# Kernel optimization log

Measured on AMD Instinct MI355X. Metric: run time of the kernel, lower is better.

The kernel has to match this reference:

```python
import jax, jax.numpy as jnp
import numpy as np

K = 3
OFFSET_SCALE = 0.25
GN_GROUPS = 8
GN_EPS = 1e-5


def setup_inputs() -> dict:
    key = jax.random.key(0)
    k1, k2, k3 = jax.random.split(key, 3)
    N, C, H, W = 4, 128, 96, 96
    Cout = 128
    x = jax.random.normal(k1, (N, C, H, W), dtype=jnp.float32)
    # offset head: small random weights so offsets are modest (tanh tames anyway)
    w_head = jax.random.normal(k2, (3, C, 3, 3), dtype=jnp.float32) * 0.05
    b_head = jnp.zeros((3,), dtype=jnp.float32)
    # kaiming-ish scale for the deform conv weight: sqrt(2 / fan_out)
    w_dcn = jax.random.normal(k3, (Cout, C, 3, 3), dtype=jnp.float32) * np.sqrt(2.0 / (Cout * 9))
    gn_gamma = jnp.ones((Cout,), dtype=jnp.float32)
    gn_beta = jnp.zeros((Cout,), dtype=jnp.float32)
    return {"x": x, "w_head": w_head, "b_head": b_head, "w_dcn": w_dcn,
            "gn_gamma": gn_gamma, "gn_beta": gn_beta}


def _conv3x3(x, w, b):
    y = jax.lax.conv_general_dilated(
        x, w, window_strides=(1, 1), padding=((1, 1), (1, 1)),
        dimension_numbers=("NCHW", "OIHW", "NCHW"))
    return y + b[None, :, None, None]


def _deform_sample(xn, py, px):
    # xn: (C,H,W); py/px: (9,H,W) absolute sampling coords (y=row, x=col)
    C, H, W = xn.shape
    y0 = jnp.floor(py).astype(jnp.int32)
    x0 = jnp.floor(px).astype(jnp.int32)
    fy = py - y0
    fx = px - x0
    xf = xn.reshape(C, H * W)

    def corner(yi, xi, wgt):
        valid = (yi >= 0) & (yi < H) & (xi >= 0) & (xi < W)
        idx = jnp.clip(yi, 0, H - 1) * W + jnp.clip(xi, 0, W - 1)  # (9,H,W)
        v = xf[:, idx.reshape(-1)].reshape(C, *idx.shape)  # (C,9,H,W)
        return v * (wgt * valid)[None]

    return (corner(y0, x0, (1 - fy) * (1 - fx))
            + corner(y0, x0 + 1, (1 - fy) * fx)
            + corner(y0 + 1, x0, fy * (1 - fx))
            + corner(y0 + 1, x0 + 1, fy * fx))


def reference(x, w_head, b_head, w_dcn, gn_gamma, gn_beta):
    N, C, H, W = x.shape
    Cout = w_dcn.shape[0]
    stride, pad, dil = 1, 1, 1

    head = _conv3x3(x, w_head, b_head)                 # (N,3,H,W)
    dx, dy, m = head[:, :1], head[:, 1:2], head[:, 2:3]
    mask = jax.nn.sigmoid(m)                           # (N,1,H,W) broadcast over 9 taps
    dx = OFFSET_SCALE * jnp.tanh(dx)
    dy = OFFSET_SCALE * jnp.tanh(dy)

    # serpentine 18-channel offsets, mmcv layout: (oy, ox) pairs per kernel tap
    z = jnp.zeros_like(dx)
    offs = jnp.concatenate(
        [z, z, z, dy, z, -dy, dx, z, z, z, -dx, z, dx, dy, dx, -dy, -dx, dy], axis=1)
    offs = offs.reshape(N, 9, 2, H, W)
    oy, ox = offs[:, :, 0], offs[:, :, 1]              # (N,9,H,W)

    ky = jnp.arange(9) // 3
    kx = jnp.arange(9) % 3
    base_y = (jnp.arange(H) * stride - pad)[None, :, None] + (ky * dil)[:, None, None]
    base_x = (jnp.arange(W) * stride - pad)[None, None, :] + (kx * dil)[:, None, None]
    py = base_y[None] + oy                             # (N,9,H,W)
    px = base_x[None] + ox

    sampled = jax.vmap(_deform_sample)(x, py, px)      # (N,C,9,H,W)
    sampled = sampled * mask[:, None]                  # modulated

    y = jnp.einsum('nckhw,ock->nohw', sampled, w_dcn.reshape(Cout, C, 9))

    # GroupNorm(8, Cout) + ReLU
    G = min(GN_GROUPS, Cout)
    yg = y.reshape(N, G, Cout // G, H, W)
    mu = yg.mean(axis=(2, 3, 4), keepdims=True)
    var = yg.var(axis=(2, 3, 4), keepdims=True)
    yn = ((yg - mu) * jax.lax.rsqrt(var + GN_EPS)).reshape(N, Cout, H, W)
    yn = yn * gn_gamma[None, :, None, None] + gn_beta[None, :, None, None]
    return jax.nn.relu(yn)
```

## Files before the change

kernel.cpp:

```cpp
#include <hip/hip_runtime.h>
#include <hip/hip_bf16.h>
#include <math.h>

#define NB   4
#define CIN  128
#define HH   96
#define WW   96
#define HWN  (HH*WW)
#define NHW  (NB*HWN)
#define COUT 128
#define KW   9
#define KDIM (CIN*KW)
#define GSZ  16
#define PXB  32
#define NBLK (NHW/PXB)

typedef __attribute__((ext_vector_type(8))) short bf16x8;
typedef __attribute__((ext_vector_type(4))) float f32x4;

#define OFF_WAH   0
#define OFF_DX    147456
#define OFF_DY    184320
#define OFF_MASK  221184
#define OFF_GN    258048
#define OFF_MAP   258240
#define OFF_PAIR  258496

__device__ __forceinline__ ushort f2bf(float f) {
    union { float f; uint u; } v; v.f = f;
    uint r = v.u + 0x7fffu + ((v.u >> 16) & 1u);
    return (ushort)(r >> 16);
}
__device__ __forceinline__ float bf2f(ushort h) {
    union { uint u; float f; } v; v.u = ((uint)h) << 16;
    return v.f;
}

__device__ __forceinline__ void barrier_keep_vm() {
    asm volatile("s_waitcnt lgkmcnt(0)\n\ts_barrier" ::: "memory");
}

__global__ __launch_bounds__(256) void pre_kernel(const float* __restrict__ x,
                                                  const float* __restrict__ w_head,
                                                  const float* __restrict__ b_head,
                                                  const float* __restrict__ wd,
                                                  ushort* __restrict__ wah,
                                                  float* __restrict__ dxv,
                                                  float* __restrict__ dyv,
                                                  float* __restrict__ maskv,
                                                  float* __restrict__ gn_part,
                                                  int* __restrict__ map,
                                                  int* __restrict__ pairB) {
    __shared__ float wl[3456];
    __shared__ float sp[4][64][3];
    const int b = blockIdx.x, t = threadIdx.x;

    if (b >= 576) {
        const int bb = b - 576;
        int i = bb * 256 + t;
        {
            int e  = i & 7;
            int l  = (i >> 3) & 63;
            int ot = (i >> 9) & 7;
            int q  = (i >> 12) & 3;
            int k  = i >> 14;
            int o  = ot * 16 + (l & 15);
            int c  = q * 32 + (l >> 4) * 8 + e;
            wah[i] = f2bf(wd[o * KDIM + c * KW + k]);
        }
        if (bb == 0 && t < 128) gn_part[t] = 0.f;
        if (bb == 0 && t < 64) {
            int l = t;
            bf16x8 A1 = {}, B1 = {}, A2 = {}, B2 = {};
            if ((l >> 4) == 0) {
                A1[0] = (short)f2bf((float)((l & 15) + 1));
                B1[0] = (short)f2bf(1.0f);
                A2[0] = (short)f2bf(1.0f);
                B2[0] = (short)f2bf((float)((l & 15) + 1));
            }
            f32x4 d1 = {0.f,0.f,0.f,0.f}, d2 = {0.f,0.f,0.f,0.f};
            d1 = __builtin_amdgcn_mfma_f32_16x16x32_bf16(A1, B1, d1, 0, 0, 0);
            d2 = __builtin_amdgcn_mfma_f32_16x16x32_bf16(A2, B2, d2, 0, 0, 0);
#pragma unroll
            for (int r = 0; r < 4; ++r) {
                int m = (int)(d1[r] + 0.5f) - 1;
                int n = (int)(d2[r] + 0.5f) - 1;
                map[l * 4 + r] = (m << 4) | n;
            }
        }
        if (bb == 1 && t < 64) {
            int l = t;
            union { bf16x8 v; short a[8]; } B;
#pragma unroll
            for (int e = 0; e < 8; ++e) {
                float val = (float)(1u << (((l >> 4) * 8 + e) & 31));
                B.a[e] = (short)f2bf(val);
            }
#pragma unroll
            for (int s = 0; s < 32; ++s) {
                union { bf16x8 v; short a[8]; } A;
#pragma unroll
                for (int e = 0; e < 8; ++e) A.a[e] = 0;
                if ((l >> 4) == (s >> 3)) A.a[s & 7] = (short)f2bf(1.0f);
                f32x4 d = {0.f, 0.f, 0.f, 0.f};
                d = __builtin_amdgcn_mfma_f32_16x16x32_bf16(A.v, B.v, d, 0, 0, 0);
                float v0 = d[0];
                if (l == 0 && v0 > 0.f) {
                    int ex; frexpf(v0, &ex);
                    int j = ex - 1;
                    if (j >= 0 && j < 32) pairB[j] = s;
                }
            }
        }
        return;
    }

    for (int i = t; i < 3456; i += 256) {
        int j = i / KDIM, r = i - j * KDIM;
        wl[r * 3 + j] = w_head[i];
    }
    __syncthreads();

    int lane = t & 63, cg = t >> 6;
    int p = b * 64 + lane;
    int n = p / HWN, hw = p % HWN;
    int h = hw / WW, w = hw % WW;

    int   offs[9];
    float msk[9];
#pragma unroll
    for (int ky = 0; ky < 3; ky++)
#pragma unroll
        for (int kx = 0; kx < 3; kx++) {
            int yy = h - 1 + ky, xx = w - 1 + kx;
            bool ok = (yy >= 0) && (yy < HH) && (xx >= 0) && (xx < WW);
            int yc = min(max(yy, 0), HH - 1), xc = min(max(xx, 0), WW - 1);
            offs[ky * 3 + kx] = yc * WW + xc;
            msk[ky * 3 + kx] = ok ? 1.f : 0.f;
        }

    float a0 = 0.f, a1 = 0.f, a2 = 0.f;
    const float* xn = x + (size_t)n * CIN * HWN;
    for (int c = cg * 32; c < cg * 32 + 32; c++) {
        const float* xc = xn + c * HWN;
        const float* wc = &wl[c * 27];
#pragma unroll
        for (int kk = 0; kk < 9; kk++) {
            float v = xc[offs[kk]] * msk[kk];
            a0 = fmaf(v, wc[kk * 3 + 0], a0);
            a1 = fmaf(v, wc[kk * 3 + 1], a1);
            a2 = fmaf(v, wc[kk * 3 + 2], a2);
        }
    }
    sp[cg][lane][0] = a0; sp[cg][lane][1] = a1; sp[cg][lane][2] = a2;
    __syncthreads();
    if (t < 64) {
        float b0 = sp[0][t][0] + sp[1][t][0] + sp[2][t][0] + sp[3][t][0] + b_head[0];
        float b1 = sp[0][t][1] + sp[1][t][1] + sp[2][t][1] + sp[3][t][1] + b_head[1];
        float b2 = sp[0][t][2] + sp[1][t][2] + sp[2][t][2] + sp[3][t][2] + b_head[2];
        int pp = b * 64 + t;
        dxv[pp]   = 0.25f * tanhf(b0);
        dyv[pp]   = 0.25f * tanhf(b1);
        maskv[pp] = 1.f / (1.f + expf(-b2));
    }
}

__global__ __launch_bounds__(256) void dcn_kernel(const float* __restrict__ x,
                                                  const ushort* __restrict__ wah,
                                                  const float* __restrict__ dxv,
                                                  const float* __restrict__ dyv,
                                                  const float* __restrict__ maskv,
                                                  const int* __restrict__ map,
                                                  const int* __restrict__ pairB,
                                                  float* __restrict__ out,
                                                  float* __restrict__ gn_part) {
    __shared__ __attribute__((aligned(16))) ushort sBh[2][4 * PXB * 8];
    __shared__ float sMask[PXB];
    __shared__ float gred[16];

    const int t = threadIdx.x;
    const int lane = t & 63;
    const int wv = t >> 6;
    const int lg = lane >> 4;
    const int ml = lane & 15;
    const int pix = t & 31;
    const int sg  = t >> 5;

    int b = blockIdx.x;
    int nb = (b & 7) * (NBLK / 8) + (b >> 3);
    const int p0  = nb * PXB;
    const int n   = p0 / HWN;
    const int hw0 = p0 % HWN;
    const float* xn = x + (size_t)n * CIN * HWN;

    if (t < PXB) sMask[t] = maskv[p0 + t];
    if (t < 16) gred[t] = 0.f;

    const float dxl = dxv[p0 + pix];
    const float dyl = dyv[p0 + pix];
    const int hme = (hw0 + pix) / WW;
    const int wme = (hw0 + pix) % WW;

    int chn[4];
#pragma unroll
    for (int e = 0; e < 4; ++e) chn[e] = pairB[sg * 4 + e] & 31;

    f32x4 acc[2][2];
#pragma unroll
    for (int i = 0; i < 2; i++)
#pragma unroll
        for (int j = 0; j < 2; j++) acc[i][j] = (f32x4){0.f, 0.f, 0.f, 0.f};

    const int oyc[9] = {0, 0, 0, 1, 0, -1, 1, 1, -1};
    const int oxc[9] = {0, 1, -1, 0, 0, 0, 1, -1, 1};
    const int ncl[9] = {1, 2, 2, 2, 1, 2, 4, 4, 4};

    int aa[4]; float wq[4];
    float raw[4][4];
    bf16x8 An0, An1;

    {
        float py = (float)(hme - 1), px = (float)(wme - 1);
        float fy0 = floorf(py), fx0 = floorf(px);
        int y0 = (int)fy0, x0 = (int)fx0;
        float fy = py - fy0, fx = px - fx0;
#pragma unroll
        for (int j = 0; j < 4; ++j) {
            int yy = y0 + (j >> 1), xx = x0 + (j & 1);
            float wb = ((j >> 1) ? fy : 1.f - fy) * ((j & 1) ? fx : 1.f - fx);
            bool ok = (yy >= 0) && (yy < HH) && (xx >= 0) && (xx < WW);
            aa[j] = min(max(yy, 0), HH - 1) * WW + min(max(xx, 0), WW - 1);
            wq[j] = ok ? wb : 0.f;
        }
#pragma unroll
        for (int e = 0; e < 4; ++e) raw[e][0] = xn[(size_t)chn[e] * HWN + aa[0]];
        const size_t abase = (size_t)(wv * 2) * 512 + lane * 8;
        An0 = *(const bf16x8*)(wah + abase);
        An1 = *(const bf16x8*)(wah + abase + 512);
    }

#pragma unroll
    for (int j = 0; j < 36; ++j) {
        const int k = j >> 2;
        const int NC = ncl[k];
        bf16x8 Ah0 = An0, Ah1 = An1;
        union { short4 v; ushort u[4]; } hv;
#pragma unroll
        for (int e = 0; e < 4; ++e) {
            float s = raw[e][0] * wq[0];
            if (NC >= 2) s += raw[e][1] * wq[1];
            if (NC == 4) s += raw[e][2] * wq[2] + raw[e][3] * wq[3];
            hv.u[e] = f2bf(s);
        }
        const int wbase = ((sg >> 1) * PXB + pix) * 8 + (sg & 1) * 4;
        *(short4*)&sBh[j & 1][wbase] = hv.v;
        if (j < 35) {
            const int jn = j + 1, kn = jn >> 2, qn = jn & 3;
            if (qn == 0) {
                const int ky = kn / 3, kx = kn - ky * 3;
                float py = (float)(hme - 1 + ky) + (float)oyc[kn] * dxl;
                float px = (float)(wme - 1 + kx) + (float)oxc[kn] * dyl;
                float fy0 = floorf(py), fx0 = floorf(px);
                int y0 = (int)fy0, x0 = (int)fx0;
                float fy = py - fy0, fx = px - fx0;
#pragma unroll
                for (int jj = 0; jj < 4; ++jj) {
                    int yy = y0 + (jj >> 1), xx = x0 + (jj & 1);
                    float wb = ((jj >> 1) ? fy : 1.f - fy) * ((jj & 1) ? fx : 1.f - fx);
                    bool ok = (yy >= 0) && (yy < HH) && (xx >= 0) && (xx < WW);
                    aa[jj] = min(max(yy, 0), HH - 1) * WW + min(max(xx, 0), WW - 1);
                    wq[jj] = ok ? wb : 0.f;
                }
                if (ncl[kn] == 2 && oxc[kn] == 0) { aa[1] = aa[2]; wq[1] = wq[2]; }
            }
            const int NCn = ncl[kn];
            const int ccn = qn * 32;
#pragma unroll
            for (int e = 0; e < 4; ++e) {
                const float* xc = xn + (size_t)(ccn + chn[e]) * HWN;
                raw[e][0] = xc[aa[0]];
                if (NCn >= 2) raw[e][1] = xc[aa[1]];
                if (NCn == 4) { raw[e][2] = xc[aa[2]]; raw[e][3] = xc[aa[3]]; }
            }
            const size_t abase = (size_t)((kn * 4 + qn) * 8 + wv * 2) * 512 + lane * 8;
            An0 = *(const bf16x8*)(wah + abase);
            An1 = *(const bf16x8*)(wah + abase + 512);
        }
        barrier_keep_vm();
#pragma unroll
        for (int pt = 0; pt < 2; ++pt) {
            const int rbase = (lg * PXB + pt * 16 + ml) * 8;
            bf16x8 Bh = *(const bf16x8*)&sBh[j & 1][rbase];
            acc[0][pt] = __builtin_amdgcn_mfma_f32_16x16x32_bf16(Ah0, Bh, acc[0][pt], 0, 0, 0);
            acc[1][pt] = __builtin_amdgcn_mfma_f32_16x16x32_bf16(Ah1, Bh, acc[1][pt], 0, 0, 0);
        }
    }

    int4 mn4 = *(const int4*)&map[lane * 4];
    int mn[4] = {mn4.x, mn4.y, mn4.z, mn4.w};
    float s1g[2] = {0.f, 0.f}, s2g[2] = {0.f, 0.f};
#pragma unroll
    for (int ot = 0; ot < 2; ++ot) {
        int otile = wv * 32 + ot * 16;
#pragma unroll
        for (int pt = 0; pt < 2; ++pt) {
#pragma unroll
            for (int r = 0; r < 4; ++r) {
                int m = mn[r] >> 4, nn2 = mn[r] & 15;
                int p = pt * 16 + nn2;
                float v = acc[ot][pt][r] * sMask[p];
                s1g[ot] += v;
                s2g[ot] += v * v;
                out[((size_t)n * COUT + otile + m) * HWN + hw0 + p] = v;
            }
        }
    }
#pragma unroll
    for (int ot = 0; ot < 2; ++ot) {
        int g = wv * 2 + ot;
        atomicAdd(&gred[g * 2 + 0], s1g[ot]);
        atomicAdd(&gred[g * 2 + 1], s2g[ot]);
    }
    __syncthreads();
    if (t < 8) {
        atomicAdd(&gn_part[n * 8 + t],      gred[t * 2 + 0]);
        atomicAdd(&gn_part[64 + n * 8 + t], gred[t * 2 + 1]);
    }
}

__global__ __launch_bounds__(256) void gn_apply(float* __restrict__ out,
                                                const float* __restrict__ gn_part,
                                                const float* __restrict__ gamma,
                                                const float* __restrict__ beta) {
    int i4 = blockIdx.x * 256 + threadIdx.x;
    size_t e = (size_t)i4 * 4;
    int og = (int)(e / HWN);
    int n = og >> 7, o = og & 127;
    int s = n * 8 + (o >> 4);
    const float cnt = (float)GSZ * (float)HWN;
    float s1 = gn_part[s], s2 = gn_part[64 + s];
    float mu = s1 / cnt;
    float var = s2 / cnt - mu * mu;
    float inv = rsqrtf(var + 1e-5f);
    float ga = gamma[o] * inv;
    float be = beta[o] - mu * ga;
    float4 v = *(float4*)(out + e);
    v.x = fmaxf(fmaf(v.x, ga, be), 0.f);
    v.y = fmaxf(fmaf(v.y, ga, be), 0.f);
    v.z = fmaxf(fmaf(v.z, ga, be), 0.f);
    v.w = fmaxf(fmaf(v.w, ga, be), 0.f);
    *(float4*)(out + e) = v;
}

extern "C" void kernel_launch(void* const* d_in, const int* in_sizes, int n_in,
                              void* d_out, int out_size, void* d_ws, size_t ws_size,
                              hipStream_t stream) {
    const float* x       = (const float*)d_in[0];
    const float* w_head  = (const float*)d_in[1];
    const float* b_head  = (const float*)d_in[2];
    const float* w_dcn   = (const float*)d_in[3];
    const float* gamma   = (const float*)d_in[4];
    const float* beta    = (const float*)d_in[5];
    float* out = (float*)d_out;
    float* ws  = (float*)d_ws;

    ushort* wah    = (ushort*)(ws + OFF_WAH);
    float* dxv     = ws + OFF_DX;
    float* dyv     = ws + OFF_DY;
    float* maskv   = ws + OFF_MASK;
    float* gn_part = ws + OFF_GN;
    int*   map     = (int*)(ws + OFF_MAP);
    int*   pairB   = (int*)(ws + OFF_PAIR);

    pre_kernel<<<1152, 256, 0, stream>>>(x, w_head, b_head, w_dcn, wah,
                                         dxv, dyv, maskv, gn_part, map, pairB);
    dcn_kernel<<<NBLK, 256, 0, stream>>>(x, wah, dxv, dyv, maskv, map, pairB, out, gn_part);
    gn_apply<<<(NB * COUT * HWN) / 4 / 256, 256, 0, stream>>>(out, gn_part, gamma, beta);
}
```

Before: 181.4 us.

## Fuse offset-head conv into DCN kernel and halve pixel tile to 16

Moves the 3-channel offset/mask head convolution out of the pre-kernel and into the deformable conv kernel, so each block computes dx, dy and mask for its own 16 pixels in shared memory. This removes the global round-trip of the offset buffers and the dependency between the two kernels. The pixel tile per block drops from 32 to 16, which doubles the block count and halves the MFMA work per block. In exchange, every block reloads the full head weights into shared memory and does an extra reduction across 16 channel groups.

```diff
diff --git a/kernel.cpp b/kernel.cpp
--- a/kernel.cpp
+++ b/kernel.cpp
@@ -12,16 +12,13 @@
 #define KW   9
 #define KDIM (CIN*KW)
 #define GSZ  16
-#define PXB  32
+#define PXB  16
 #define NBLK (NHW/PXB)
 
 typedef __attribute__((ext_vector_type(8))) short bf16x8;
 typedef __attribute__((ext_vector_type(4))) float f32x4;
 
 #define OFF_WAH   0
-#define OFF_DX    147456
-#define OFF_DY    184320
-#define OFF_MASK  221184
 #define OFF_GN    258048
 #define OFF_MAP   258240
 #define OFF_PAIR  258496
@@ -31,160 +28,95 @@
     uint r = v.u + 0x7fffu + ((v.u >> 16) & 1u);
     return (ushort)(r >> 16);
 }
-__device__ __forceinline__ float bf2f(ushort h) {
-    union { uint u; float f; } v; v.u = ((uint)h) << 16;
-    return v.f;
-}
 
 __device__ __forceinline__ void barrier_keep_vm() {
     asm volatile("s_waitcnt lgkmcnt(0)\n\ts_barrier" ::: "memory");
 }
 
-__global__ __launch_bounds__(256) void pre_kernel(const float* __restrict__ x,
-                                                  const float* __restrict__ w_head,
-                                                  const float* __restrict__ b_head,
-                                                  const float* __restrict__ wd,
+__global__ __launch_bounds__(256) void pre_kernel(const float* __restrict__ wd,
                                                   ushort* __restrict__ wah,
-                                                  float* __restrict__ dxv,
-                                                  float* __restrict__ dyv,
-                                                  float* __restrict__ maskv,
                                                   float* __restrict__ gn_part,
                                                   int* __restrict__ map,
                                                   int* __restrict__ pairB) {
-    __shared__ float wl[3456];
-    __shared__ float sp[4][64][3];
     const int b = blockIdx.x, t = threadIdx.x;
-
-    if (b >= 576) {
-        const int bb = b - 576;
-        int i = bb * 256 + t;
-        {
-            int e  = i & 7;
-            int l  = (i >> 3) & 63;
-            int ot = (i >> 9) & 7;
-            int q  = (i >> 12) & 3;
-            int k  = i >> 14;
-            int o  = ot * 16 + (l & 15);
-            int c  = q * 32 + (l >> 4) * 8 + e;
-            wah[i] = f2bf(wd[o * KDIM + c * KW + k]);
-        }
-        if (bb == 0 && t < 128) gn_part[t] = 0.f;
-        if (bb == 0 && t < 64) {
-            int l = t;
-            bf16x8 A1 = {}, B1 = {}, A2 = {}, B2 = {};
-            if ((l >> 4) == 0) {
-                A1[0] = (short)f2bf((float)((l & 15) + 1));
-                B1[0] = (short)f2bf(1.0f);
-                A2[0] = (short)f2bf(1.0f);
-                B2[0] = (short)f2bf((float)((l & 15) + 1));
-            }
-            f32x4 d1 = {0.f,0.f,0.f,0.f}, d2 = {0.f,0.f,0.f,0.f};
-            d1 = __builtin_amdgcn_mfma_f32_16x16x32_bf16(A1, B1, d1, 0, 0, 0);
-            d2 = __builtin_amdgcn_mfma_f32_16x16x32_bf16(A2, B2, d2, 0, 0, 0);
-#pragma unroll
-            for (int r = 0; r < 4; ++r) {
-                int m = (int)(d1[r] + 0.5f) - 1;
-                int n = (int)(d2[r] + 0.5f) - 1;
-                map[l * 4 + r] = (m << 4) | n;
-            }
-        }
-        if (bb == 1 && t < 64) {
-            int l = t;
-            union { bf16x8 v; short a[8]; } B;
-#pragma unroll
-            for (int e = 0; e < 8; ++e) {
-                float val = (float)(1u << (((l >> 4) * 8 + e) & 31));
-                B.a[e] = (short)f2bf(val);
-            }
-#pragma unroll
-            for (int s = 0; s < 32; ++s) {
-                union { bf16x8 v; short a[8]; } A;
-#pragma unroll
-                for (int e = 0; e < 8; ++e) A.a[e] = 0;
-                if ((l >> 4) == (s >> 3)) A.a[s & 7] = (short)f2bf(1.0f);
-                f32x4 d = {0.f, 0.f, 0.f, 0.f};
-                d = __builtin_amdgcn_mfma_f32_16x16x32_bf16(A.v, B.v, d, 0, 0, 0);
-                float v0 = d[0];
-                if (l == 0 && v0 > 0.f) {
-                    int ex; frexpf(v0, &ex);
-                    int j = ex - 1;
-                    if (j >= 0 && j < 32) pairB[j] = s;
-                }
-            }
-        }
-        return;
-    }
-
-    for (int i = t; i < 3456; i += 256) {
-        int j = i / KDIM, r = i - j * KDIM;
-        wl[r * 3 + j] = w_head[i];
-    }
-    __syncthreads();
-
-    int lane = t & 63, cg = t >> 6;
-    int p = b * 64 + lane;
-    int n = p / HWN, hw = p % HWN;
-    int h = hw / WW, w = hw % WW;
-
-    int   offs[9];
-    float msk[9];
-#pragma unroll
-    for (int ky = 0; ky < 3; ky++)
-#pragma unroll
-        for (int kx = 0; kx < 3; kx++) {
-            int yy = h - 1 + ky, xx = w - 1 + kx;
-            bool ok = (yy >= 0) && (yy < HH) && (xx >= 0) && (xx < WW);
-            int yc = min(max(yy, 0), HH - 1), xc = min(max(xx, 0), WW - 1);
-            offs[ky * 3 + kx] = yc * WW + xc;
-            msk[ky * 3 + kx] = ok ? 1.f : 0.f;
-        }
-
-    float a0 = 0.f, a1 = 0.f, a2 = 0.f;
-    const float* xn = x + (size_t)n * CIN * HWN;
-    for (int c = cg * 32; c < cg * 32 + 32; c++) {
-        const float* xc = xn + c * HWN;
-        const float* wc = &wl[c * 27];
-#pragma unroll
-        for (int kk = 0; kk < 9; kk++) {
-            float v = xc[offs[kk]] * msk[kk];
-            a0 = fmaf(v, wc[kk * 3 + 0], a0);
-            a1 = fmaf(v, wc[kk * 3 + 1], a1);
-            a2 = fmaf(v, wc[kk * 3 + 2], a2);
-        }
-    }
-    sp[cg][lane][0] = a0; sp[cg][lane][1] = a1; sp[cg][lane][2] = a2;
-    __syncthreads();
-    if (t < 64) {
-        float b0 = sp[0][t][0] + sp[1][t][0] + sp[2][t][0] + sp[3][t][0] + b_head[0];
-        float b1 = sp[0][t][1] + sp[1][t][1] + sp[2][t][1] + sp[3][t][1] + b_head[1];
-        float b2 = sp[0][t][2] + sp[1][t][2] + sp[2][t][2] + sp[3][t][2] + b_head[2];
-        int pp = b * 64 + t;
-        dxv[pp]   = 0.25f * tanhf(b0);
-        dyv[pp]   = 0.25f * tanhf(b1);
-        maskv[pp] = 1.f / (1.f + expf(-b2));
+    int i = b * 256 + t;
+    {
+        int e  = i & 7;
+        int l  = (i >> 3) & 63;
+        int ot = (i >> 9) & 7;
+        int q  = (i >> 12) & 3;
+        int k  = i >> 14;
+        int o  = ot * 16 + (l & 15);
+        int c  = q * 32 + (l >> 4) * 8 + e;
+        wah[i] = f2bf(wd[o * KDIM + c * KW + k]);
+    }
+    if (b == 0 && t < 128) gn_part[t] = 0.f;
+    if (b == 0 && t < 64) {
+        int l = t;
+        bf16x8 A1 = {}, B1 = {}, A2 = {}, B2 = {};
+        if ((l >> 4) == 0) {
+            A1[0] = (short)f2bf((float)((l & 15) + 1));
+            B1[0] = (short)f2bf(1.0f);
+            A2[0] = (short)f2bf(1.0f);
+            B2[0] = (short)f2bf((float)((l & 15) + 1));
+        }
+        f32x4 d1 = {0.f,0.f,0.f,0.f}, d2 = {0.f,0.f,0.f,0.f};
+        d1 = __builtin_amdgcn_mfma_f32_16x16x32_bf16(A1, B1, d1, 0, 0, 0);
+        d2 = __builtin_amdgcn_mfma_f32_16x16x32_bf16(A2, B2, d2, 0, 0, 0);
+#pragma unroll
+        for (int r = 0; r < 4; ++r) {
+            int m = (int)(d1[r] + 0.5f) - 1;
+            int n = (int)(d2[r] + 0.5f) - 1;
+            map[l * 4 + r] = (m << 4) | n;
+        }
+    }
+    if (b == 1 && t < 64) {
+        int l = t;
+        union { bf16x8 v; short a[8]; } B;
+#pragma unroll
+        for (int e = 0; e < 8; ++e) {
+            float val = (float)(1u << (((l >> 4) * 8 + e) & 31));
+            B.a[e] = (short)f2bf(val);
+        }
+#pragma unroll
+        for (int s = 0; s < 32; ++s) {
+            union { bf16x8 v; short a[8]; } A;
+#pragma unroll
+            for (int e = 0; e < 8; ++e) A.a[e] = 0;
+            if ((l >> 4) == (s >> 3)) A.a[s & 7] = (short)f2bf(1.0f);
+            f32x4 d = {0.f, 0.f, 0.f, 0.f};
+            d = __builtin_amdgcn_mfma_f32_16x16x32_bf16(A.v, B.v, d, 0, 0, 0);
+            float v0 = d[0];
+            if (l == 0 && v0 > 0.f) {
+                int ex; frexpf(v0, &ex);
+                int j = ex - 1;
+                if (j >= 0 && j < 32) pairB[j] = s;
+            }
+        }
     }
 }
 
 __global__ __launch_bounds__(256) void dcn_kernel(const float* __restrict__ x,
+                                                  const float* __restrict__ w_head,
+                                                  const float* __restrict__ b_head,
                                                   const ushort* __restrict__ wah,
-                                                  const float* __restrict__ dxv,
-                                                  const float* __restrict__ dyv,
-                                                  const float* __restrict__ maskv,
                                                   const int* __restrict__ map,
                                                   const int* __restrict__ pairB,
                                                   float* __restrict__ out,
                                                   float* __restrict__ gn_part) {
-    __shared__ __attribute__((aligned(16))) ushort sBh[2][4 * PXB * 8];
-    __shared__ float sMask[PXB];
-    __shared__ float gred[16];
+    __shared__ __attribute__((aligned(16))) char smem[16896];
+    __shared__ float sDx[16], sDy[16], sMask[16], gred[16];
+    float* wl = (float*)smem;
+    float* sp = (float*)(smem + 13824);
+    ushort* sB = (ushort*)smem;
 
     const int t = threadIdx.x;
     const int lane = t & 63;
     const int wv = t >> 6;
     const int lg = lane >> 4;
     const int ml = lane & 15;
-    const int pix = t & 31;
-    const int sg  = t >> 5;
+    const int pix = t & 15;
+    const int sg  = t >> 4;
 
     int b = blockIdx.x;
     int nb = (b & 7) * (NBLK / 8) + (b >> 3);
@@ -193,30 +125,77 @@
     const int hw0 = p0 % HWN;
     const float* xn = x + (size_t)n * CIN * HWN;
 
-    if (t < PXB) sMask[t] = maskv[p0 + t];
     if (t < 16) gred[t] = 0.f;
 
-    const float dxl = dxv[p0 + pix];
-    const float dyl = dyv[p0 + pix];
     const int hme = (hw0 + pix) / WW;
     const int wme = (hw0 + pix) % WW;
 
-    int chn[4];
-#pragma unroll
-    for (int e = 0; e < 4; ++e) chn[e] = pairB[sg * 4 + e] & 31;
-
-    f32x4 acc[2][2];
-#pragma unroll
-    for (int i = 0; i < 2; i++)
-#pragma unroll
-        for (int j = 0; j < 2; j++) acc[i][j] = (f32x4){0.f, 0.f, 0.f, 0.f};
+    for (int i = t; i < 3456; i += 256) {
+        int j = i / KDIM, r = i - j * KDIM;
+        wl[r * 3 + j] = w_head[i];
+    }
+    __syncthreads();
+    {
+        int   offs[9];
+        float msk[9];
+#pragma unroll
+        for (int ky = 0; ky < 3; ky++)
+#pragma unroll
+            for (int kx = 0; kx < 3; kx++) {
+                int yy = hme - 1 + ky, xx = wme - 1 + kx;
+                bool ok = (yy >= 0) && (yy < HH) && (xx >= 0) && (xx < WW);
+                int yc = min(max(yy, 0), HH - 1), xc = min(max(xx, 0), WW - 1);
+                offs[ky * 3 + kx] = yc * WW + xc;
+                msk[ky * 3 + kx] = ok ? 1.f : 0.f;
+            }
+        float a0 = 0.f, a1 = 0.f, a2 = 0.f;
+        for (int c = sg * 8; c < sg * 8 + 8; c++) {
+            const float* xc = xn + (size_t)c * HWN;
+            const float* wc = &wl[c * 27];
+#pragma unroll
+            for (int kk = 0; kk < 9; kk++) {
+                float v = xc[offs[kk]] * msk[kk];
+                a0 = fmaf(v, wc[kk * 3 + 0], a0);
+                a1 = fmaf(v, wc[kk * 3 + 1], a1);
+                a2 = fmaf(v, wc[kk * 3 + 2], a2);
+            }
+        }
+        sp[(sg * 16 + pix) * 3 + 0] = a0;
+        sp[(sg * 16 + pix) * 3 + 1] = a1;
+        sp[(sg * 16 + pix) * 3 + 2] = a2;
+    }
+    __syncthreads();
+    if (t < 16) {
+        float b0 = b_head[0], b1 = b_head[1], b2 = b_head[2];
+#pragma unroll
+        for (int cg = 0; cg < 16; ++cg) {
+            b0 += sp[(cg * 16 + t) * 3 + 0];
+            b1 += sp[(cg * 16 + t) * 3 + 1];
+            b2 += sp[(cg * 16 + t) * 3 + 2];
+        }
+        sDx[t]   = 0.25f * tanhf(b0);
+        sDy[t]   = 0.25f * tanhf(b1);
+        sMask[t] = 1.f / (1.f + expf(-b2));
+    }
+    __syncthreads();
+
+    const float dxl = sDx[pix];
+    const float dyl = sDy[pix];
+
+    int chn[2];
+#pragma unroll
+    for (int h = 0; h < 2; ++h) chn[h] = pairB[sg * 2 + h] & 31;
+
+    f32x4 acc[2];
+#pragma unroll
+    for (int i = 0; i < 2; i++) acc[i] = (f32x4){0.f, 0.f, 0.f, 0.f};
 
     const int oyc[9] = {0, 0, 0, 1, 0, -1, 1, 1, -1};
     const int oxc[9] = {0, 1, -1, 0, 0, 0, 1, -1, 1};
     const int ncl[9] = {1, 2, 2, 2, 1, 2, 4, 4, 4};
 
     int aa[4]; float wq[4];
-    float raw[4][4];
+    float raw[2][4];
     bf16x8 An0, An1;
 
     {
@@ -233,7 +212,7 @@
             wq[j] = ok ? wb : 0.f;
         }
 #pragma unroll
-        for (int e = 0; e < 4; ++e) raw[e][0] = xn[(size_t)chn[e] * HWN + aa[0]];
+        for (int h = 0; h < 2; ++h) raw[h][0] = xn[(size_t)chn[h] * HWN + aa[0]];
         const size_t abase = (size_t)(wv * 2) * 512 + lane * 8;
         An0 = *(const bf16x8*)(wah + abase);
         An1 = *(const bf16x8*)(wah + abase + 512);
@@ -244,16 +223,16 @@
         const int k = j >> 2;
         const int NC = ncl[k];
         bf16x8 Ah0 = An0, Ah1 = An1;
-        union { short4 v; ushort u[4]; } hv;
-#pragma unroll
-        for (int e = 0; e < 4; ++e) {
-            float s = raw[e][0] * wq[0];
-            if (NC >= 2) s += raw[e][1] * wq[1];
-            if (NC == 4) s += raw[e][2] * wq[2] + raw[e][3] * wq[3];
-            hv.u[e] = f2bf(s);
-        }
-        const int wbase = ((sg >> 1) * PXB + pix) * 8 + (sg & 1) * 4;
-        *(short4*)&sBh[j & 1][wbase] = hv.v;
+        union { ushort u[2]; uint v; } hv;
+#pragma unroll
+        for (int h = 0; h < 2; ++h) {
+            float s = raw[h][0] * wq[0];
+            if (NC >= 2) s += raw[h][1] * wq[1];
+            if (NC == 4) s += raw[h][2] * wq[2] + raw[h][3] * wq[3];
+            hv.u[h] = f2bf(s);
+        }
+        const int wbase = (j & 1) * 512 + ((sg >> 2) * 16 + pix) * 8 + (sg & 3) * 2;
+        *(uint*)&sB[wbase] = hv.v;
         if (j < 35) {
             const int jn = j + 1, kn = jn >> 2, qn = jn & 3;
             if (qn == 0) {
@@ -276,24 +255,21 @@
             const int NCn = ncl[kn];
             const int ccn = qn * 32;
 #pragma unroll
-            for (int e = 0; e < 4; ++e) {
-                const float* xc = xn + (size_t)(ccn + chn[e]) * HWN;
-                raw[e][0] = xc[aa[0]];
-                if (NCn >= 2) raw[e][1] = xc[aa[1]];
-                if (NCn == 4) { raw[e][2] = xc[aa[2]]; raw[e][3] = xc[aa[3]]; }
+            for (int h = 0; h < 2; ++h) {
+                const float* xc = xn + (size_t)(ccn + chn[h]) * HWN;
+                raw[h][0] = xc[aa[0]];
+                if (NCn >= 2) raw[h][1] = xc[aa[1]];
+                if (NCn == 4) { raw[h][2] = xc[aa[2]]; raw[h][3] = xc[aa[3]]; }
             }
             const size_t abase = (size_t)((kn * 4 + qn) * 8 + wv * 2) * 512 + lane * 8;
             An0 = *(const bf16x8*)(wah + abase);
             An1 = *(const bf16x8*)(wah + abase + 512);
         }
         barrier_keep_vm();
-#pragma unroll
-        for (int pt = 0; pt < 2; ++pt) {
-            const int rbase = (lg * PXB + pt * 16 + ml) * 8;
-            bf16x8 Bh = *(const bf16x8*)&sBh[j & 1][rbase];
-            acc[0][pt] = __builtin_amdgcn_mfma_f32_16x16x32_bf16(Ah0, Bh, acc[0][pt], 0, 0, 0);
-            acc[1][pt] = __builtin_amdgcn_mfma_f32_16x16x32_bf16(Ah1, Bh, acc[1][pt], 0, 0, 0);
-        }
+        const int rbase = (j & 1) * 512 + (lg * 16 + ml) * 8;
+        bf16x8 Bh = *(const bf16x8*)&sB[rbase];
+        acc[0] = __builtin_amdgcn_mfma_f32_16x16x32_bf16(Ah0, Bh, acc[0], 0, 0, 0);
+        acc[1] = __builtin_amdgcn_mfma_f32_16x16x32_bf16(Ah1, Bh, acc[1], 0, 0, 0);
     }
 
     int4 mn4 = *(const int4*)&map[lane * 4];
@@ -303,16 +279,12 @@
     for (int ot = 0; ot < 2; ++ot) {
         int otile = wv * 32 + ot * 16;
 #pragma unroll
-        for (int pt = 0; pt < 2; ++pt) {
-#pragma unroll
-            for (int r = 0; r < 4; ++r) {
-                int m = mn[r] >> 4, nn2 = mn[r] & 15;
-                int p = pt * 16 + nn2;
-                float v = acc[ot][pt][r] * sMask[p];
-                s1g[ot] += v;
-                s2g[ot] += v * v;
-                out[((size_t)n * COUT + otile + m) * HWN + hw0 + p] = v;
-            }
+        for (int r = 0; r < 4; ++r) {
+            int m = mn[r] >> 4, nn2 = mn[r] & 15;
+            float v = acc[ot][r] * sMask[nn2];
+            s1g[ot] += v;
+            s2g[ot] += v * v;
+            out[((size_t)n * COUT + otile + m) * HWN + hw0 + nn2] = v;
         }
     }
 #pragma unroll
@@ -365,15 +337,11 @@
     float* ws  = (float*)d_ws;
 
     ushort* wah    = (ushort*)(ws + OFF_WAH);
-    float* dxv     = ws + OFF_DX;
-    float* dyv     = ws + OFF_DY;
-    float* maskv   = ws + OFF_MASK;
     float* gn_part = ws + OFF_GN;
     int*   map     = (int*)(ws + OFF_MAP);
     int*   pairB   = (int*)(ws + OFF_PAIR);
 
-    pre_kernel<<<1152, 256, 0, stream>>>(x, w_head, b_head, w_dcn, wah,
-                                         dxv, dyv, maskv, gn_part, map, pairB);
-    dcn_kernel<<<NBLK, 256, 0, stream>>>(x, wah, dxv, dyv, maskv, map, pairB, out, gn_part);
+    pre_kernel<<<576, 256, 0, stream>>>(w_dcn, wah, gn_part, map, pairB);
+    dcn_kernel<<<NBLK, 256, 0, stream>>>(x, w_head, b_head, wah, map, pairB, out, gn_part);
     gn_apply<<<(NB * COUT * HWN) / 4 / 256, 256, 0, stream>>>(out, gn_part, gamma, beta);
 }
```

Measured after the change: 192.2 us. 5.9% more time.
